# Kernel optimization log

Hardware: AMD Instinct MI355X
Metric: run time of the kernel (lower is better)

## Reference

```python
import jax, jax.numpy as jnp
import numpy as np

N = 16384      # total nodes (B graphs x 64 squares)
B = 256        # number of graphs
NODES = 64     # nodes per graph (chess board)
E = 131072     # directed edges (avg degree 8)
F_IN = 128
H = 256
GH = 4         # GAT heads
TH = 8         # transformer heads
L_GNN = 8
L_TF = 6
EPS = 1e-5


def layer_norm(x, g, b):
    m = jnp.mean(x, -1, keepdims=True)
    v = jnp.mean((x - m) ** 2, -1, keepdims=True)
    return (x - m) * jax.lax.rsqrt(v + EPS) * g + b


def setup_inputs() -> dict:
    key = jax.random.key(0)
    ks = iter(jax.random.split(key, 80))

    def nrm(shape, s=0.02):
        return jax.random.normal(next(ks), shape, jnp.float32) * s

    x = jax.random.normal(next(ks), (N, F_IN), jnp.float32)
    gid = jax.random.randint(next(ks), (E,), 0, B)
    off = jax.random.randint(next(ks), (2, E), 0, NODES)
    edge_index = gid[None, :] * NODES + off          # edges stay within a graph
    batch = jnp.arange(N, dtype=jnp.int32) // NODES
    piece_types = jax.random.randint(next(ks), (N,), 1, 7)
    return dict(
        x=x, edge_index=edge_index, batch=batch, piece_types=piece_types,
        emb_w=nrm((H, F_IN)), emb_b=nrm((H,)),
        gat_w=nrm((L_GNN, GH * H, H)), gat_as=nrm((L_GNN, GH, H)),
        gat_ad=nrm((L_GNN, GH, H)), gat_b=nrm((L_GNN, H)),
        gnn_g=jnp.ones((L_GNN, H)), gnn_beta=jnp.zeros((L_GNN, H)),
        ln1_g=jnp.ones((L_TF, H)), ln1_b=jnp.zeros((L_TF, H)),
        in_w=nrm((L_TF, 3 * H, H)), in_b=nrm((L_TF, 3 * H)),
        out_w=nrm((L_TF, H, H)), out_b=nrm((L_TF, H)),
        ln2_g=jnp.ones((L_TF, H)), ln2_b=jnp.zeros((L_TF, H)),
        ff1_w=nrm((L_TF, 4 * H, H)), ff1_b=nrm((L_TF, 4 * H)),
        ff2_w=nrm((L_TF, H, 4 * H)), ff2_b=nrm((L_TF, H)),
        pool_w=nrm((H,)), pool_b=nrm((1,)),
        vw1=nrm((H, H)), vb1=nrm((H,)), vw2=nrm((1, H)), vb2=nrm((1,)),
        pw1=nrm((H, H)), pb1=nrm((H,)), pw2=nrm((H, H)), pb2=nrm((H,)),
        uw1=nrm((H // 2, H)), ub1=nrm((H // 2,)), uw2=nrm((1, H // 2)), ub2=nrm((1,)))


def _forward(x, edge_index, batch, emb_w, emb_b, gat_w, gat_as, gat_ad, gat_b,
             gnn_g, gnn_beta, ln1_g, ln1_b, in_w, in_b, out_w, out_b, ln2_g,
             ln2_b, ff1_w, ff1_b, ff2_w, ff2_b, pool_w, pool_b, vw1, vb1, vw2,
             vb2, pw1, pb1, pw2, pb2, uw1, ub1, uw2, ub2):
    loops = jnp.arange(N, dtype=edge_index.dtype)     # GATConv add_self_loops=True
    src = jnp.concatenate([edge_index[0], loops])
    dst = jnp.concatenate([edge_index[1], loops])
    h = x @ emb_w.T + emb_b                           # [N,H] node embedding

    def gnn_layer(h, p):                              # ResidualGNNLayer
        W, a_s, a_d, bias, g, beta = p
        hp = (h @ W.T).reshape(N, GH, H)              # per-head projection
        al_s = jnp.sum(hp * a_s, -1)                  # [N,GH]
        al_d = jnp.sum(hp * a_d, -1)
        e = jax.nn.leaky_relu(al_s[src] + al_d[dst], 0.2)
        m = jax.ops.segment_max(e, dst, num_segments=N)
        ex = jnp.exp(e - m[dst])                      # segment softmax over dst
        den = jax.ops.segment_sum(ex, dst, num_segments=N)
        alpha = ex / den[dst]
        out = jax.ops.segment_sum(hp[src] * alpha[:, :, None], dst, num_segments=N)
        out = out.mean(1) + bias                      # concat=False -> head mean
        out = jax.nn.gelu(layer_norm(out, g, beta), approximate=False)
        return h + out, None                          # project = Identity

    h, _ = jax.lax.scan(gnn_layer, h, (gat_w, gat_as, gat_ad, gat_b, gnn_g, gnn_beta))

    # nn.MultiheadAttention defaults batch_first=False: axis0 (=B graphs) is the
    # sequence axis, axis1 (=64 nodes) is the batch axis — faithful to the source.
    xt = h.reshape(B, NODES, H)
    HD = H // TH

    def tf_layer(t, p):
        g1, b1, iw, ib, ow, ob, g2, b2, w1, fb1, w2, fb2 = p
        tn = layer_norm(t, g1, b1)
        q, k, v = jnp.split(tn @ iw.T + ib, 3, axis=-1)
        q = q.reshape(B, NODES, TH, HD)
        k = k.reshape(B, NODES, TH, HD)
        v = v.reshape(B, NODES, TH, HD)
        att = jnp.einsum('sbhd,tbhd->bhst', q, k) * (1.0 / HD ** 0.5)
        att = jax.nn.softmax(att, -1)
        o = jnp.einsum('bhst,tbhd->sbhd', att, v).reshape(B, NODES, H)
        t = t + (o @ ow.T + ob)
        tn = layer_norm(t, g2, b2)
        ff = jax.nn.gelu(tn @ w1.T + fb1, approximate=False) @ w2.T + fb2
        return t + ff, None

    xt, _ = jax.lax.scan(tf_layer, xt, (ln1_g, ln1_b, in_w, in_b, out_w, out_b,
                                        ln2_g, ln2_b, ff1_w, ff1_b, ff2_w, ff2_b))
    h = xt.reshape(N, H)

    # global attention pooling: softmax over ALL nodes (dim=0, as in the source)
    aw = jax.nn.softmax(h @ pool_w + pool_b[0], axis=0)
    g_rep = jax.ops.segment_sum(h * aw[:, None], batch, num_segments=B)
    value = jnp.tanh(jax.nn.gelu(g_rep @ vw1.T + vb1, approximate=False) @ vw2.T + vb2)[:, 0]
    policy = jax.nn.gelu(h @ pw1.T + pb1, approximate=False) @ pw2.T + pb2
    unc = jax.nn.softplus(jax.nn.gelu(g_rep @ uw1.T + ub1, approximate=False) @ uw2.T + ub2)[:, 0]
    return value, policy, unc


def reference(x, edge_index, batch, piece_types, emb_w, emb_b, gat_w, gat_as,
              gat_ad, gat_b, gnn_g, gnn_beta, ln1_g, ln1_b, in_w, in_b, out_w,
              out_b, ln2_g, ln2_b, ff1_w, ff1_b, ff2_w, ff2_b, pool_w, pool_b,
              vw1, vb1, vw2, vb2, pw1, pb1, pw2, pb2, uw1, ub1, uw2, ub2):
    # piece_types feeds PositionSpecificFeatureExtractor whose output is dead
    # code in the source forward (never used), so it is omitted here.
    return _forward(x, edge_index, batch, emb_w, emb_b, gat_w, gat_as, gat_ad,
                    gat_b, gnn_g, gnn_beta, ln1_g, ln1_b, in_w, in_b, out_w,
                    out_b, ln2_g, ln2_b, ff1_w, ff1_b, ff2_w, ff2_b, pool_w,
                    pool_b, vw1, vb1, vw2, vb2, pw1, pb1, pw2, pb2, uw1, ub1,
                    uw2, ub2)
```

## Files before the change

kernel.cpp:

```cpp
#include <hip/hip_runtime.h>
#include <hip/hip_bf16.h>

typedef __hip_bfloat16 bf16;
typedef __bf16 bf16x8 __attribute__((ext_vector_type(8)));
typedef float  f32x4  __attribute__((ext_vector_type(4)));

#define N_NODES 16384
#define HDIM    256
#define NE      131072
#define NE2     147456

__device__ __forceinline__ float b2f(bf16 v){ return __bfloat162float(v); }
__device__ __forceinline__ bf16  f2b(float v){ return __float2bfloat16(v); }
__device__ __forceinline__ float us2f(unsigned short u){
  union { unsigned int i; float f; } c; c.i = ((unsigned int)u) << 16; return c.f;
}
__device__ __forceinline__ unsigned short f2us(float f){
  bf16 h = __float2bfloat16(f);
  unsigned short u; __builtin_memcpy(&u, &h, 2); return u;
}
__device__ __forceinline__ float gelu_f(float x){
  return 0.5f * x * (1.0f + erff(x * 0.7071067811865476f));
}
__device__ __forceinline__ float wave_sum(float v){
  #pragma unroll
  for (int o = 32; o > 0; o >>= 1) v += __shfl_xor(v, o);
  return v;
}
__device__ __forceinline__ float wave_max(float v){
  #pragma unroll
  for (int o = 32; o > 0; o >>= 1) v = fmaxf(v, __shfl_xor(v, o));
  return v;
}

__device__ __forceinline__ float4 load4(const float* p){ return *(const float4*)p; }
__device__ __forceinline__ float4 load4(const bf16* p){
  ushort4 u = *(const ushort4*)p;
  return make_float4(us2f(u.x), us2f(u.y), us2f(u.z), us2f(u.w));
}
__device__ __forceinline__ void store4(float* p, float4 v){ *(float4*)p = v; }
__device__ __forceinline__ void store4(bf16* p, float4 v){
  ushort4 u = make_ushort4(f2us(v.x), f2us(v.y), f2us(v.z), f2us(v.w));
  *(ushort4*)p = u;
}
__device__ __forceinline__ void storev(float* p, float4 v){ *(float4*)p = v; }
__device__ __forceinline__ void storev(bf16*  p, float4 v){ store4(p, v); }

__device__ __forceinline__ void async_ld16(const bf16* g, unsigned short* l){
  __builtin_amdgcn_global_load_lds(
      (const __attribute__((address_space(1))) void*)g,
      (__attribute__((address_space(3))) void*)l, 16, 0, 0);
}

__global__ void detect_dtype(const unsigned short* __restrict__ x, int n, int* __restrict__ flags){
  int i = blockIdx.x * 256 + threadIdx.x;
  if (i < n) {
    unsigned short u = x[i];
    if ((u & 0x7F80) == 0x7F80) atomicOr(&flags[1], 1);
  }
}
struct ConvArgs {
  const void* src[35];
  unsigned short* dst[35];
  int cumg[36];
  int n[35];
};
__global__ void conv_all4(ConvArgs a, const int* __restrict__ flags){
  int gi = blockIdx.x * 256 + threadIdx.x;
  if (gi >= a.cumg[35]) return;
  int lo = 0, hi = 34;
  while (lo < hi) { int mid = (lo + hi + 1) >> 1; if (gi >= a.cumg[mid]) lo = mid; else hi = mid - 1; }
  int e0 = (gi - a.cumg[lo]) << 2;
  int n = a.n[lo];
  unsigned short* d = a.dst[lo];
  if (flags[1]) {
    const float* s = (const float*)a.src[lo];
    if (e0 + 4 <= n) {
      float4 v = *(const float4*)(s + e0);
      *(ushort4*)(d + e0) = make_ushort4(f2us(v.x), f2us(v.y), f2us(v.z), f2us(v.w));
    } else {
      for (int t = 0; t < n - e0; ++t) d[e0 + t] = f2us(s[e0 + t]);
    }
  } else {
    const unsigned short* s = (const unsigned short*)a.src[lo];
    if (e0 + 4 <= n) *(ushort4*)(d + e0) = *(const ushort4*)(s + e0);
    else for (int t = 0; t < n - e0; ++t) d[e0 + t] = s[e0 + t];
  }
}
__global__ void emit_out(const unsigned short* __restrict__ stage, void* __restrict__ out,
                         int n, const int* __restrict__ flags){
  int i = blockIdx.x * 256 + threadIdx.x;
  if (i >= n) return;
  if (flags[1]) ((float*)out)[i] = us2f(stage[i]);
  else          ((unsigned short*)out)[i] = stage[i];
}
__global__ void write_sentinel(bf16* out, float v){ out[threadIdx.x] = f2b(v); }

#define GF_GELU 1
#define GF_RES  2
#define GF_MIR  4
#define GF_ALS  8

template<typename TO, int FLAGS>
__global__ __launch_bounds__(256) void gemm2(
    const bf16* __restrict__ A, const bf16* __restrict__ W,
    const bf16* __restrict__ bias, const float* __restrict__ res,
    TO* __restrict__ C, bf16* __restrict__ C2, int M, int Nn, int K,
    const bf16* __restrict__ asp, const bf16* __restrict__ adp,
    float* __restrict__ alsp)
{
  __shared__ __align__(16) char ldsraw[36864];
  unsigned short* sA = (unsigned short*)ldsraw;
  unsigned short* sB = sA + 128 * 64;
  const int tid = threadIdx.x;
  const int wave = tid >> 6, lane = tid & 63;
  const int quad = lane >> 4, l16 = lane & 15;
  const int wm = wave & 1, wn = wave >> 1;
  const int row0 = blockIdx.y << 7, col0 = blockIdx.x << 7;
  const int lr = lane >> 3, lc = lane & 7;

  f32x4 acc[4][4] = {};

  for (int kt = 0; kt < K; kt += 64) {
    #pragma unroll
    for (int it = 0; it < 4; ++it) {
      int r0 = (wave << 5) + (it << 3);
      int rr = r0 + lr;
      int gch = lc ^ (rr & 7);
      async_ld16(A + (size_t)(row0 + rr) * K + kt + (gch << 3), sA + (r0 << 6));
      async_ld16(W + (size_t)(col0 + rr) * K + kt + (gch << 3), sB + (r0 << 6));
    }
    __syncthreads();
    #pragma unroll
    for (int kk = 0; kk < 2; ++kk) {
      bf16x8 af[4];
      #pragma unroll
      for (int i = 0; i < 4; ++i) {
        int m = (wm << 6) + (i << 4) + l16;
        af[i] = *(const bf16x8*)&sA[(m << 6) + ((((kk << 2) + quad) ^ (l16 & 7)) << 3)];
      }
      #pragma unroll
      for (int j = 0; j < 4; ++j) {
        int n = (wn << 6) + (j << 4) + l16;
        bf16x8 bfr = *(const bf16x8*)&sB[(n << 6) + ((((kk << 2) + quad) ^ (l16 & 7)) << 3)];
        #pragma unroll
        for (int i = 0; i < 4; ++i)
          acc[i][j] = __builtin_amdgcn_mfma_f32_16x16x32_bf16(af[i], bfr, acc[i][j], 0, 0, 0);
      }
    }
    __syncthreads();
  }

  float* ct = (float*)ldsraw + wave * (64 * 36);
  #pragma unroll
  for (int p = 0; p < 2; ++p) {
    #pragma unroll
    for (int i = 0; i < 4; ++i)
      #pragma unroll
      for (int r = 0; r < 4; ++r) {
        int row = (i << 4) + (quad << 2) + r;
        ct[row * 36 + l16]      = acc[i][(p << 1) + 0][r];
        ct[row * 36 + 16 + l16] = acc[i][(p << 1) + 1][r];
      }
    float4 sS = make_float4(0.f, 0.f, 0.f, 0.f);
    float4 sD = make_float4(0.f, 0.f, 0.f, 0.f);
    #pragma unroll
    for (int it2 = 0; it2 < 8; ++it2) {
      int row = (it2 << 3) + lr;
      int c4 = lc << 2;
      float4 v = *(const float4*)&ct[row * 36 + c4];
      int gcol = col0 + (wn << 6) + (p << 5) + c4;
      size_t gidx = (size_t)(row0 + (wm << 6) + row) * Nn + gcol;
      if (FLAGS & GF_ALS) {
        float asv = b2f(asp[row0 + (wm << 6) + row]);
        float adv = b2f(adp[row0 + (wm << 6) + row]);
        sS.x += asv * v.x; sS.y += asv * v.y; sS.z += asv * v.z; sS.w += asv * v.w;
        sD.x += adv * v.x; sD.y += adv * v.y; sD.z += adv * v.z; sD.w += adv * v.w;
      }
      if (bias) {
        float4 bv = load4(bias + gcol);
        v.x += bv.x; v.y += bv.y; v.z += bv.z; v.w += bv.w;
      }
      if (FLAGS & GF_GELU) {
        v.x = gelu_f(v.x); v.y = gelu_f(v.y); v.z = gelu_f(v.z); v.w = gelu_f(v.w);
      }
      if (FLAGS & GF_RES) {
        float4 rv = *(const float4*)&res[gidx];
        v.x += rv.x; v.y += rv.y; v.z += rv.z; v.w += rv.w;
      }
      storev(C + gidx, v);
      if (FLAGS & GF_MIR) store4(C2 + gidx, v);
    }
    if (FLAGS & GF_ALS) {
      #pragma unroll
      for (int o = 8; o < 64; o <<= 1) {
        sS.x += __shfl_xor(sS.x, o); sS.y += __shfl_xor(sS.y, o);
        sS.z += __shfl_xor(sS.z, o); sS.w += __shfl_xor(sS.w, o);
        sD.x += __shfl_xor(sD.x, o); sD.y += __shfl_xor(sD.y, o);
        sD.z += __shfl_xor(sD.z, o); sD.w += __shfl_xor(sD.w, o);
      }
      if (lr == 0) {
        int node = col0 + (wn << 6) + (p << 5) + (lc << 2);
        int hd2 = blockIdx.y >> 1;
        int slice = ((blockIdx.y & 1) << 1) | wm;
        *(float4*)&alsp[(size_t)((slice << 3) + hd2) * Nn + node] = sS;
        *(float4*)&alsp[(size_t)((slice << 3) + 4 + hd2) * Nn + node] = sD;
      }
    }
  }
}

template<bool POOL>
__global__ __launch_bounds__(256) void gemm_rln(
    const bf16* __restrict__ A, const bf16* __restrict__ W,
    const bf16* __restrict__ bias, float* __restrict__ h,
    bf16* __restrict__ tn, const bf16* __restrict__ lng,
    const bf16* __restrict__ lnb, int K,
    bf16* __restrict__ hbm, const bf16* __restrict__ pw,
    const bf16* __restrict__ pbp, float* __restrict__ logits)
{
  __shared__ __align__(16) char ldsraw[36864];
  unsigned short* sA = (unsigned short*)ldsraw;
  unsigned short* sB = sA + 32 * 64;
  const int tid = threadIdx.x;
  const int wave = tid >> 6, lane = tid & 63;
  const int quad = lane >> 4, l16 = lane & 15;
  const int row0 = blockIdx.x << 5;
  const int lr = lane >> 3, lc = lane & 7;

  f32x4 acc[2][4] = {};

  for (int kt = 0; kt < K; kt += 64) {
    {
      int rr = (wave << 3) + lr;
      int gch = lc ^ (rr & 7);
      async_ld16(A + (size_t)(row0 + rr) * K + kt + (gch << 3), sA + (wave << 9));
    }
    #pragma unroll
    for (int it = 0; it < 8; ++it) {
      int r0 = (wave << 6) + (it << 3);
      int rr = r0 + lr;
      int gch = lc ^ (rr & 7);
      async_ld16(W + (size_t)rr * K + kt + (gch << 3), sB + (r0 << 6));
    }
    __syncthreads();
    #pragma unroll
    for (int kk = 0; kk < 2; ++kk) {
      bf16x8 af[2];
      #pragma unroll
      for (int i = 0; i < 2; ++i) {
        int m = (i << 4) + l16;
        af[i] = *(const bf16x8*)&sA[(m << 6) + ((((kk << 2) + quad) ^ (l16 & 7)) << 3)];
      }
      #pragma unroll
      for (int j = 0; j < 4; ++j) {
        int n = (wave << 6) + (j << 4) + l16;
        bf16x8 bfr = *(const bf16x8*)&sB[(n << 6) + ((((kk << 2) + quad) ^ (l16 & 7)) << 3)];
        #pragma unroll
        for (int i = 0; i < 2; ++i)
          acc[i][j] = __builtin_amdgcn_mfma_f32_16x16x32_bf16(af[i], bfr, acc[i][j], 0, 0, 0);
      }
    }
    __syncthreads();
  }

  float* ct = (float*)ldsraw;
  #pragma unroll
  for (int j = 0; j < 4; ++j) {
    int col = (wave << 6) + (j << 4) + l16;
    #pragma unroll
    for (int i = 0; i < 2; ++i)
      #pragma unroll
      for (int r = 0; r < 4; ++r)
        ct[((i << 4) + (quad << 2) + r) * 260 + col] = acc[i][j][r];
  }
  __syncthreads();

  const int row = tid >> 3, q = tid & 7;
  const int c0 = q << 5;
  size_t gr = (size_t)(row0 + row) * 256 + c0;
  float4 v[8];
  float s1 = 0.f;
  #pragma unroll
  for (int k = 0; k < 8; ++k) {
    float4 cv = *(const float4*)&ct[row * 260 + c0 + (k << 2)];
    float4 bv = load4(bias + c0 + (k << 2));
    float4 rv = *(const float4*)&h[gr + (k << 2)];
    v[k].x = cv.x + bv.x + rv.x;
    v[k].y = cv.y + bv.y + rv.y;
    v[k].z = cv.z + bv.z + rv.z;
    v[k].w = cv.w + bv.w + rv.w;
    *(float4*)&h[gr + (k << 2)] = v[k];
    if (POOL) store4(hbm + gr + (k << 2), v[k]);
    s1 += v[k].x + v[k].y + v[k].z + v[k].w;
  }
  if (POOL) {
    float dp = 0.f;
    #pragma unroll
    for (int k = 0; k < 8; ++k) {
      float4 wv = load4(pw + c0 + (k << 2));
      dp += v[k].x * wv.x + v[k].y * wv.y + v[k].z * wv.z + v[k].w * wv.w;
    }
    dp += __shfl_xor(dp, 1); dp += __shfl_xor(dp, 2); dp += __shfl_xor(dp, 4);
    if (q == 0) logits[row0 + row] = dp + b2f(pbp[0]);
  } else {
    s1 += __shfl_xor(s1, 1); s1 += __shfl_xor(s1, 2); s1 += __shfl_xor(s1, 4);
    float mean = s1 * (1.0f / 256.0f);
    float s2 = 0.f;
    #pragma unroll
    for (int k = 0; k < 8; ++k) {
      float dx = v[k].x - mean, dy = v[k].y - mean, dz = v[k].z - mean, dw = v[k].w - mean;
      s2 += dx * dx + dy * dy + dz * dz + dw * dw;
    }
    s2 += __shfl_xor(s2, 1); s2 += __shfl_xor(s2, 2); s2 += __shfl_xor(s2, 4);
    float rstd = rsqrtf(s2 * (1.0f / 256.0f) + 1e-5f);
    #pragma unroll
    for (int k = 0; k < 8; ++k) {
      float4 gv = load4(lng + c0 + (k << 2));
      float4 bv2 = load4(lnb + c0 + (k << 2));
      float4 y;
      y.x = (v[k].x - mean) * rstd * gv.x + bv2.x;
      y.y = (v[k].y - mean) * rstd * gv.y + bv2.y;
      y.z = (v[k].z - mean) * rstd * gv.z + bv2.z;
      y.w = (v[k].w - mean) * rstd * gv.w + bv2.w;
      store4(tn + gr + (k << 2), y);
    }
  }
}

__global__ void csr_count(const int* __restrict__ edst, int* __restrict__ cnt){
  int e = blockIdx.x * 256 + threadIdx.x;
  if (e < NE2) {
    int d = (e < NE) ? edst[e] : (e - NE);
    atomicAdd(&cnt[d], 1);
  }
}
__global__ __launch_bounds__(1024) void csr_scan(const int* __restrict__ cnt, int* __restrict__ off){
  __shared__ int ls[1024];
  int t = threadIdx.x;
  int base = t * 16;
  int loc[16]; int s = 0;
  #pragma unroll
  for (int j = 0; j < 16; ++j) { loc[j] = s; s += cnt[base + j]; }
  ls[t] = s;
  __syncthreads();
  for (int o = 1; o < 1024; o <<= 1) {
    int v = (t >= o) ? ls[t - o] : 0;
    __syncthreads();
    ls[t] += v;
    __syncthreads();
  }
  int pre = (t == 0) ? 0 : ls[t - 1];
  #pragma unroll
  for (int j = 0; j < 16; ++j) off[base + j] = pre + loc[j];
  if (t == 1023) off[N_NODES] = ls[1023];
}
__global__ void csr_fill(const int* __restrict__ edst, const int* __restrict__ off,
                         int* __restrict__ fillc, int* __restrict__ list){
  int e = blockIdx.x * 256 + threadIdx.x;
  if (e < NE2) {
    int d = (e < NE) ? edst[e] : (e - NE);
    int p = atomicAdd(&fillc[d], 1);
    list[off[d] + p] = e;
  }
}

#define ALF_S 68

__device__ __forceinline__ bf16x8 pack8(const float* v, float scale){
  unsigned short u[8];
  #pragma unroll
  for (int t = 0; t < 8; ++t) u[t] = f2us(v[t] * scale);
  bf16x8 r; __builtin_memcpy(&r, u, 16); return r;
}

__global__ __launch_bounds__(256) void gat_graph2(
    const int* __restrict__ esrc, const bf16* __restrict__ hpT_g,
    const int* __restrict__ off, const int* __restrict__ list,
    const float* __restrict__ alsp,
    bf16* __restrict__ msg4, int g0, int hn)
{
  __shared__ unsigned short hpT[256 * 64];
  __shared__ float alpha[64 * ALF_S];
  __shared__ float als[64], ald[64], dinv[64];

  const int hd = blockIdx.x & 3;
  const int lg = blockIdx.x >> 2;
  const int g  = g0 + lg;
  const int tid = threadIdx.x;
  const int wave = tid >> 6, lane = tid & 63;
  const int quad = lane >> 4, l16 = lane & 15;
  const int nd = tid >> 2;
  const int k4 = tid & 3;

  {
    const int rl = lane >> 3, jj = lane & 7;
    #pragma unroll
    for (int it = 0; it < 8; ++it) {
      int c = (it << 5) + (wave << 3) + rl;
      async_ld16(hpT_g + (size_t)((hd << 8) + c) * 16384 + (g << 6) + ((jj ^ (c & 7)) << 3),
                 hpT + (((it << 5) + (wave << 3)) << 6));
    }
  }
  if (tid < 128) {
    int n2 = tid & 63;
    int sd = (tid >> 6) << 2;
    float v = 0.f;
    #pragma unroll
    for (int sl = 0; sl < 4; ++sl)
      v += alsp[(size_t)((sl << 3) + sd + hd) * 16384 + (g << 6) + n2];
    if (sd) ald[n2] = v; else als[n2] = v;
  }
  #pragma unroll
  for (int idx = tid; idx < 64 * ALF_S; idx += 256) alpha[idx] = 0.f;
  __syncthreads();

  {
    int st = off[(g << 6) + nd];
    int deg = off[(g << 6) + nd + 1] - st;
    float ad = ald[nd];
    float mx = -1e30f;
    for (int e = k4; e < deg; e += 4) {
      int ed = list[st + e];
      int sl = ((ed < NE) ? esrc[ed] : (ed - NE)) - (g << 6);
      float v = als[sl] + ad;
      v = (v > 0.f) ? v : 0.2f * v;
      mx = fmaxf(mx, v);
    }
    mx = fmaxf(mx, __shfl_xor(mx, 1)); mx = fmaxf(mx, __shfl_xor(mx, 2));
    float den = 0.f;
    for (int e = k4; e < deg; e += 4) {
      int ed = list[st + e];
      int sl = ((ed < NE) ? esrc[ed] : (ed - NE)) - (g << 6);
      float v = als[sl] + ad;
      v = (v > 0.f) ? v : 0.2f * v;
      float w = __expf(v - mx);
      den += w;
      atomicAdd(&alpha[nd * ALF_S + sl], w);
    }
    den += __shfl_xor(den, 1); den += __shfl_xor(den, 2);
    if (k4 == 0) dinv[nd] = 1.0f / den;
  }
  __syncthreads();

  f32x4 acc[4][4] = {};
  #pragma unroll
  for (int kk = 0; kk < 2; ++kk) {
    bf16x8 af[4];
    #pragma unroll
    for (int i = 0; i < 4; ++i) {
      int m = (i << 4) + l16;
      const float* ap = &alpha[m * ALF_S + (kk << 5) + (quad << 3)];
      float av[8];
      float4 a0 = *(const float4*)ap, a1 = *(const float4*)(ap + 4);
      av[0]=a0.x; av[1]=a0.y; av[2]=a0.z; av[3]=a0.w;
      av[4]=a1.x; av[5]=a1.y; av[6]=a1.z; av[7]=a1.w;
      af[i] = pack8(av, dinv[m]);
    }
    #pragma unroll
    for (int j = 0; j < 4; ++j) {
      int c2 = (wave << 6) + (j << 4) + l16;
      int chunk = (kk << 2) + quad;
      bf16x8 bfr = *(const bf16x8*)&hpT[(c2 << 6) + ((chunk ^ (c2 & 7)) << 3)];
      #pragma unroll
      for (int i = 0; i < 4; ++i)
        acc[i][j] = __builtin_amdgcn_mfma_f32_16x16x32_bf16(af[i], bfr, acc[i][j], 0, 0, 0);
    }
  }

  #pragma unroll
  for (int j = 0; j < 4; ++j) {
    int col = (wave << 6) + (j << 4) + l16;
    #pragma unroll
    for (int i = 0; i < 4; ++i) {
      int rbase = (i << 4) + (quad << 2);
      #pragma unroll
      for (int r = 0; r < 4; ++r)
        msg4[((size_t)hd * hn + (lg << 6) + rbase + r) * 256 + col] = f2b(acc[i][j][r]);
    }
  }
}

__global__ __launch_bounds__(256) void gat_epi(
    const bf16* __restrict__ msg4, int hn, int n0,
    const bf16* __restrict__ bias, const bf16* __restrict__ gg, const bf16* __restrict__ gb,
    float* __restrict__ h, bf16* __restrict__ hb,
    const bf16* __restrict__ lng, const bf16* __restrict__ lnb, bf16* __restrict__ tno)
{
  int nl = blockIdx.x * 4 + (threadIdx.x >> 6);
  int lane = threadIdx.x & 63;
  int c = lane * 4;
  float4 s = make_float4(0.f, 0.f, 0.f, 0.f);
  #pragma unroll
  for (int hd = 0; hd < 4; ++hd) {
    float4 m = load4(msg4 + ((size_t)hd * hn + nl) * 256 + c);
    s.x += m.x; s.y += m.y; s.z += m.z; s.w += m.w;
  }
  float4 bv = load4(bias + c);
  float ox = s.x * 0.25f + bv.x, oy = s.y * 0.25f + bv.y;
  float oz = s.z * 0.25f + bv.z, ow = s.w * 0.25f + bv.w;
  float mean = wave_sum(ox + oy + oz + ow) * (1.0f / 256.0f);
  float dx = ox - mean, dy = oy - mean, dz = oz - mean, dw = ow - mean;
  float var = wave_sum(dx*dx + dy*dy + dz*dz + dw*dw) * (1.0f / 256.0f);
  float r = rsqrtf(var + 1e-5f);
  float4 gv = load4(gg + c); float4 b2 = load4(gb + c);
  size_t base = ((size_t)(n0 + nl)) * 256 + c;
  float4 hv = load4(h + base);
  hv.x += gelu_f(dx * r * gv.x + b2.x);
  hv.y += gelu_f(dy * r * gv.y + b2.y);
  hv.z += gelu_f(dz * r * gv.z + b2.z);
  hv.w += gelu_f(dw * r * gv.w + b2.w);
  store4(h + base, hv);
  store4(hb + base, hv);
  if (lng) {
    float m2 = wave_sum(hv.x + hv.y + hv.z + hv.w) * (1.0f / 256.0f);
    float ex = hv.x - m2, ey = hv.y - m2, ez = hv.z - m2, ew = hv.w - m2;
    float v2 = wave_sum(ex*ex + ey*ey + ez*ez + ew*ew) * (1.0f / 256.0f);
    float r2 = rsqrtf(v2 + 1e-5f);
    float4 g2 = load4(lng + c); float4 bb = load4(lnb + c);
    store4(tno + base, make_float4(ex*r2*g2.x + bb.x, ey*r2*g2.y + bb.y,
                                   ez*r2*g2.z + bb.z, ew*r2*g2.w + bb.w));
  }
}

__global__ __launch_bounds__(256) void ln_kernel(
    const float* __restrict__ x, bf16* __restrict__ y,
    const bf16* __restrict__ g, const bf16* __restrict__ b)
{
  int row = blockIdx.x * 4 + (threadIdx.x >> 6);
  int lane = threadIdx.x & 63;
  int c = lane * 4;
  float4 v = load4(x + (size_t)row * 256 + c);
  float mean = wave_sum(v.x + v.y + v.z + v.w) * (1.0f / 256.0f);
  float dx = v.x - mean, dy = v.y - mean, dz = v.z - mean, dw = v.w - mean;
  float var = wave_sum(dx*dx + dy*dy + dz*dz + dw*dw) * (1.0f / 256.0f);
  float r = rsqrtf(var + 1e-5f);
  float4 gv = load4(g + c); float4 bv = load4(b + c);
  store4(y + (size_t)row * 256 + c,
         make_float4(dx*r*gv.x + bv.x, dy*r*gv.y + bv.y, dz*r*gv.z + bv.z, dw*r*gv.w + bv.w));
}

#define VT_LDS 268
#define P_LDS  72

__global__ __launch_bounds__(256) void attn_mfma(
    const bf16* __restrict__ qkv, bf16* __restrict__ obuf)
{
  const int b  = blockIdx.x & 63;
  const int hh = blockIdx.x >> 6;
  __shared__ unsigned short VTs[32 * VT_LDS];
  __shared__ unsigned short Ps[4][64 * P_LDS];
  const int tid  = threadIdx.x;
  const int wave = tid >> 6, lane = tid & 63;
  const int quad = lane >> 4, l16 = lane & 15;

  {
    const bf16* vb = qkv + (size_t)(tid * 64 + b) * 768 + 512 + hh * 32;
    unsigned short vv[32];
    *(uint4*)&vv[0]  = *(const uint4*)(vb);
    *(uint4*)&vv[8]  = *(const uint4*)(vb + 8);
    *(uint4*)&vv[16] = *(const uint4*)(vb + 16);
    *(uint4*)&vv[24] = *(const uint4*)(vb + 24);
    #pragma unroll
    for (int d = 0; d < 32; ++d) VTs[d * VT_LDS + tid] = vv[d];
  }
  bf16x8 qf[4];
  #pragma unroll
  for (int i = 0; i < 4; ++i) {
    int s = (wave << 6) + (i << 4) + l16;
    qf[i] = *(const bf16x8*)(qkv + (size_t)(s * 64 + b) * 768 + hh * 32 + (quad << 3));
  }
  __syncthreads();

  const float scale = 0.17677669529663687f;
  f32x4 oacc[4][2] = {};
  float lsum[4][4] = {};
  unsigned short* Pw = &Ps[wave][0];

  for (int nt = 0; nt < 4; ++nt) {
    bf16x8 kf[4];
    #pragma unroll
    for (int j = 0; j < 4; ++j) {
      int t = (nt << 6) + (j << 4) + l16;
      kf[j] = *(const bf16x8*)(qkv + (size_t)(t * 64 + b) * 768 + 256 + hh * 32 + (quad << 3));
    }
    f32x4 zero = {0.f, 0.f, 0.f, 0.f};
    f32x4 sx[4][4];
    #pragma unroll
    for (int i = 0; i < 4; ++i)
      #pragma unroll
      for (int j = 0; j < 4; ++j)
        sx[i][j] = __builtin_amdgcn_mfma_f32_16x16x32_bf16(qf[i], kf[j], zero, 0, 0, 0);
    #pragma unroll
    for (int i = 0; i < 4; ++i) {
      #pragma unroll
      for (int r = 0; r < 4; ++r) {
        float p[4]; float rs = 0.f;
        #pragma unroll
        for (int j = 0; j < 4; ++j) {
          float sc = fminf(fmaxf(sx[i][j][r] * scale, -60.f), 60.f);
          p[j] = __expf(sc);
          rs += p[j];
        }
        #pragma unroll
        for (int o = 1; o < 16; o <<= 1) rs += __shfl_xor(rs, o);
        lsum[i][r] += rs;
        int row = (i << 4) + (quad << 2) + r;
        #pragma unroll
        for (int j = 0; j < 4; ++j)
          Pw[row * P_LDS + (j << 4) + l16] = f2us(p[j]);
      }
    }
    #pragma unroll
    for (int kk = 0; kk < 2; ++kk) {
      bf16x8 vf[2];
      #pragma unroll
      for (int j2 = 0; j2 < 2; ++j2)
        vf[j2] = *(const bf16x8*)&VTs[((j2 << 4) + l16) * VT_LDS + (nt << 6) + (kk << 5) + (quad << 3)];
      #pragma unroll
      for (int i2 = 0; i2 < 4; ++i2) {
        bf16x8 pf = *(const bf16x8*)&Pw[((i2 << 4) + l16) * P_LDS + (kk << 5) + (quad << 3)];
        #pragma unroll
        for (int j2 = 0; j2 < 2; ++j2)
          oacc[i2][j2] = __builtin_amdgcn_mfma_f32_16x16x32_bf16(pf, vf[j2], oacc[i2][j2], 0, 0, 0);
      }
    }
  }
  #pragma unroll
  for (int i = 0; i < 4; ++i) {
    #pragma unroll
    for (int r = 0; r < 4; ++r) {
      int srow = (wave << 6) + (i << 4) + (quad << 2) + r;
      float inv = 1.0f / lsum[i][r];
      #pragma unroll
      for (int j2 = 0; j2 < 2; ++j2)
        obuf[(size_t)(srow * 64 + b) * 256 + hh * 32 + (j2 << 4) + l16] = f2b(oacc[i][j2][r] * inv);
    }
  }
}

__global__ __launch_bounds__(1024) void pool_reduce(
    const float* __restrict__ logits, float* __restrict__ red)
{
  __shared__ float sm[16];
  int t = threadIdx.x;
  float m = -1e30f;
  for (int i = t; i < N_NODES; i += 1024) m = fmaxf(m, logits[i]);
  m = wave_max(m);
  if ((t & 63) == 0) sm[t >> 6] = m;
  __syncthreads();
  if (t == 0) { float mm = sm[0]; for (int i = 1; i < 16; ++i) mm = fmaxf(mm, sm[i]); sm[0] = mm; }
  __syncthreads();
  float gmax = sm[0];
  __syncthreads();
  float s = 0.f;
  for (int i = t; i < N_NODES; i += 1024) s += expf(logits[i] - gmax);
  s = wave_sum(s);
  if ((t & 63) == 0) sm[t >> 6] = s;
  __syncthreads();
  if (t == 0) { float ss = 0.f; for (int i = 0; i < 16; ++i) ss += sm[i]; red[0] = gmax; red[1] = 1.0f / ss; }
}
__global__ __launch_bounds__(256) void pool_grep(
    const float* __restrict__ h, const float* __restrict__ logits,
    const float* __restrict__ red, bf16* __restrict__ g_rep)
{
  __shared__ float w[64];
  int g = blockIdx.x; int tid = threadIdx.x;
  if (tid < 64) w[tid] = expf(logits[g * 64 + tid] - red[0]) * red[1];
  __syncthreads();
  float acc = 0.f;
  for (int nd = 0; nd < 64; ++nd) acc += h[((size_t)g * 64 + nd) * 256 + tid] * w[nd];
  g_rep[(size_t)g * 256 + tid] = f2b(acc);
}
__global__ __launch_bounds__(256) void head_value(
    const float* __restrict__ vt, const bf16* __restrict__ w2, const bf16* __restrict__ b2,
    bf16* __restrict__ out)
{
  int gidx = blockIdx.x * 4 + (threadIdx.x >> 6); int lane = threadIdx.x & 63;
  float acc = 0.f;
  #pragma unroll
  for (int j = 0; j < 4; ++j) { int c = j * 64 + lane; acc += vt[(size_t)gidx * 256 + c] * b2f(w2[c]); }
  acc = wave_sum(acc);
  if (lane == 0) out[gidx] = f2b(tanhf(acc + b2f(b2[0])));
}
__global__ __launch_bounds__(256) void head_unc(
    const float* __restrict__ ut, const bf16* __restrict__ w2, const bf16* __restrict__ b2,
    bf16* __restrict__ out)
{
  int gidx = blockIdx.x * 4 + (threadIdx.x >> 6); int lane = threadIdx.x & 63;
  float acc = 0.f;
  #pragma unroll
  for (int j = 0; j < 2; ++j) { int c = j * 64 + lane; acc += ut[(size_t)gidx * 128 + c] * b2f(w2[c]); }
  acc = wave_sum(acc);
  if (lane == 0) {
    float x = acc + b2f(b2[0]);
    float sp = (x > 20.f) ? x : log1pf(expf(x));
    out[gidx] = f2b(sp);
  }
}

extern "C" void kernel_launch(void* const* d_in, const int* in_sizes, int n_in,
                              void* d_out, int out_size, void* d_ws, size_t ws_size,
                              hipStream_t stream)
{
  (void)out_size;
  const int* eidx = (const int*)d_in[1];

  char* ws = (char*)d_ws;
  size_t wo = 0;
  auto alloc = [&](size_t bytes) -> char* {
    char* p = ws + wo; wo += (bytes + 255) & ~(size_t)255; return p;
  };
  int*   flags = (int*)alloc(256);
  int*   cnt   = (int*)alloc((size_t)N_NODES * 4);
  int*   fillc = (int*)alloc((size_t)N_NODES * 4);
  size_t zero_end = wo;

  bf16* conv[38] = {};
  static const int fidx[35] = {0,4,5,6,7,8,9,10,11,12,13,14,15,16,17,18,19,
                               20,21,22,23,24,25,26,27,28,29,30,31,32,33,34,35,36,37};
  for (int j = 0; j < 35; ++j) {
    int idx = fidx[j];
    conv[idx] = (bf16*)alloc((size_t)in_sizes[idx] * 2);
  }
  float* h     = (float*)alloc((size_t)N_NODES * 256 * 4);
  bf16*  hb    = (bf16*) alloc((size_t)N_NODES * 256 * 2);
  bf16*  big   = (bf16*) alloc((size_t)N_NODES * 1024 * 2);
  const int OUT_ELEMS = 256 + N_NODES * 256 + 256;
  bf16*  tn     = (bf16*)alloc((size_t)N_NODES * 256 * 2);
  bf16*  ostage = (bf16*)alloc((size_t)OUT_ELEMS * 2);
  int*   off   = (int*)alloc((size_t)(N_NODES + 1) * 4);
  int*   list  = (int*)alloc((size_t)NE2 * 4);
  float* logits= (float*)alloc((size_t)N_NODES * 4);
  float* redb  = (float*)alloc(256);
  bf16*  g_rep = (bf16*)alloc((size_t)256 * 256 * 2);
  float* val_t = (float*)alloc((size_t)256 * 256 * 4);
  float* unc_t = (float*)alloc((size_t)256 * 128 * 4);
  float* alsp  = (float*)alloc((size_t)32 * N_NODES * 4);
  size_t base_needed = wo;

  if (n_in != 38)                   { write_sentinel<<<1,256,0,stream>>>((bf16*)d_out, 4.f);  return; }
  if (in_sizes[0] != N_NODES * 128) { write_sentinel<<<1,256,0,stream>>>((bf16*)d_out, 8.f);  return; }
  if (in_sizes[1] != 2 * NE)        { write_sentinel<<<1,256,0,stream>>>((bf16*)d_out, 16.f); return; }
  if (ws_size < base_needed)        { write_sentinel<<<1,256,0,stream>>>((bf16*)d_out, 32.f); return; }

  size_t msg_bytes = (size_t)4 * N_NODES * 256 * 2;
  bf16* msg4; int halves;
  if (ws_size >= base_needed + msg_bytes + 256) {
    msg4 = (bf16*)alloc(msg_bytes); halves = 1;
  } else {
    msg4 = tn; halves = 2;
  }

  hipMemsetAsync(d_ws, 0, zero_end, stream);

  detect_dtype<<<256, 256, 0, stream>>>((const unsigned short*)d_in[0], 65536, flags);
  {
    ConvArgs ca;
    int cum = 0;
    for (int j = 0; j < 35; ++j) {
      int idx = fidx[j];
      ca.src[j] = d_in[idx];
      ca.dst[j] = (unsigned short*)conv[idx];
      ca.cumg[j] = cum;
      ca.n[j] = in_sizes[idx];
      cum += (in_sizes[idx] + 3) >> 2;
    }
    ca.cumg[35] = cum;
    conv_all4<<<(cum + 255) / 256, 256, 0, stream>>>(ca, flags);
  }
  const bf16 *xb = conv[0], *emb_w = conv[4], *emb_b = conv[5], *gat_w = conv[6],
             *gat_as = conv[7], *gat_ad = conv[8], *gat_b = conv[9], *gnn_g = conv[10],
             *gnn_beta = conv[11], *ln1_g = conv[12], *ln1_b = conv[13], *in_w = conv[14],
             *in_b = conv[15], *out_w = conv[16], *out_b = conv[17], *ln2_g = conv[18],
             *ln2_b = conv[19], *ff1_w = conv[20], *ff1_b = conv[21], *ff2_w = conv[22],
             *ff2_b = conv[23], *pool_w = conv[24], *pool_b = conv[25],
             *vw1 = conv[26], *vb1 = conv[27], *vw2 = conv[28], *vb2 = conv[29],
             *pw1 = conv[30], *pb1 = conv[31], *pw2 = conv[32], *pb2 = conv[33],
             *uw1 = conv[34], *ub1 = conv[35], *uw2 = conv[36], *ub2 = conv[37];

  bf16* qkv  = big;
  bf16* obuf = big + (size_t)N_NODES * 768;
  bf16* hpT_g = big;
  bf16* ffb  = big;
  bf16* o_val = ostage;
  bf16* o_pol = ostage + 256;
  bf16* o_unc = ostage + 256 + (size_t)N_NODES * 256;

  csr_count<<<(NE2 + 255) / 256, 256, 0, stream>>>(eidx + NE, cnt);
  csr_scan<<<1, 1024, 0, stream>>>(cnt, off);
  csr_fill<<<(NE2 + 255) / 256, 256, 0, stream>>>(eidx + NE, off, fillc, list);

  gemm2<float, GF_MIR><<<dim3(2, 128), 256, 0, stream>>>(
      xb, emb_w, emb_b, nullptr, h, hb, N_NODES, 256, 128,
      nullptr, nullptr, nullptr);

  const int gph = 256 / halves;
  const int hn  = N_NODES / halves;
  for (int l = 0; l < 8; ++l) {
    gemm2<bf16, GF_ALS><<<dim3(128, 8), 256, 0, stream>>>(
        gat_w + (size_t)l * 1024 * 256, hb, nullptr, nullptr, hpT_g, nullptr,
        1024, N_NODES, 256, gat_as + l * 1024, gat_ad + l * 1024, alsp);
    const bf16* lng = (l == 7 && halves == 1) ? ln1_g : nullptr;
    const bf16* lnb = (l == 7 && halves == 1) ? ln1_b : nullptr;
    for (int ph = 0; ph < halves; ++ph) {
      gat_graph2<<<gph * 4, 256, 0, stream>>>(eidx, hpT_g, off, list, alsp,
          msg4, ph * gph, hn);
      gat_epi<<<hn / 4, 256, 0, stream>>>(msg4, hn, ph * hn,
          gat_b + l * 256, gnn_g + l * 256, gnn_beta + l * 256, h, hb,
          lng, lnb, tn);
    }
  }
  if (halves == 2)
    ln_kernel<<<N_NODES / 4, 256, 0, stream>>>(h, tn, ln1_g, ln1_b);

  for (int l = 0; l < 6; ++l) {
    gemm2<bf16, 0><<<dim3(6, 128), 256, 0, stream>>>(
        tn, in_w + (size_t)l * 768 * 256, in_b + l * 768, nullptr, qkv, nullptr, N_NODES, 768, 256,
        nullptr, nullptr, nullptr);
    attn_mfma<<<512, 256, 0, stream>>>(qkv, obuf);
    gemm_rln<false><<<N_NODES / 32, 256, 0, stream>>>(
        obuf, out_w + (size_t)l * 256 * 256, out_b + l * 256, h, tn,
        ln2_g + l * 256, ln2_b + l * 256, 256,
        nullptr, nullptr, nullptr, nullptr);
    gemm2<bf16, GF_GELU><<<dim3(8, 128), 256, 0, stream>>>(
        tn, ff1_w + (size_t)l * 1024 * 256, ff1_b + l * 1024, nullptr, ffb, nullptr, N_NODES, 1024, 256,
        nullptr, nullptr, nullptr);
    if (l < 5)
      gemm_rln<false><<<N_NODES / 32, 256, 0, stream>>>(
          ffb, ff2_w + (size_t)l * 256 * 1024, ff2_b + l * 256, h, tn,
          ln1_g + (l + 1) * 256, ln1_b + (l + 1) * 256, 1024,
          nullptr, nullptr, nullptr, nullptr);
    else
      gemm_rln<true><<<N_NODES / 32, 256, 0, stream>>>(
          ffb, ff2_w + (size_t)l * 256 * 1024, ff2_b + l * 256, h, nullptr,
          nullptr, nullptr, 1024,
          hb, pool_w, pool_b, logits);
  }

  pool_reduce<<<1, 1024, 0, stream>>>(logits, redb);
  pool_grep<<<256, 256, 0, stream>>>(h, logits, redb, g_rep);
  gemm2<float, GF_GELU><<<dim3(2, 2), 256, 0, stream>>>(
      g_rep, vw1, vb1, nullptr, val_t, nullptr, 256, 256, 256,
      nullptr, nullptr, nullptr);
  head_value<<<64, 256, 0, stream>>>(val_t, vw2, vb2, o_val);
  gemm2<float, GF_GELU><<<dim3(1, 2), 256, 0, stream>>>(
      g_rep, uw1, ub1, nullptr, unc_t, nullptr, 256, 128, 256,
      nullptr, nullptr, nullptr);
  head_unc<<<64, 256, 0, stream>>>(unc_t, uw2, ub2, o_unc);
  gemm2<bf16, GF_GELU><<<dim3(2, 128), 256, 0, stream>>>(
      hb, pw1, pb1, nullptr, tn, nullptr, N_NODES, 256, 256,
      nullptr, nullptr, nullptr);
  gemm2<bf16, 0><<<dim3(2, 128), 256, 0, stream>>>(
      tn, pw2, pb2, nullptr, o_pol, nullptr, N_NODES, 256, 256,
      nullptr, nullptr, nullptr);

  emit_out<<<(OUT_ELEMS + 255) / 256, 256, 0, stream>>>(
      (const unsigned short*)ostage, d_out, OUT_ELEMS, flags);
}
```

Measured before the change: 1.501 ms.

## Fuse policy MLP and value/uncertainty heads; remap GEMM block order

Replaces the two policy-head GEMM launches with one kernel that keeps the GELU intermediate in shared memory, so the 16384x256 intermediate no longer goes through global memory. Merges the value and uncertainty MLPs, including their final dot products, into a single small kernel, which removes four launches and two temporary buffers. Also permutes block indices in gemm2 and gemm_rln so consecutive blocks are spread across row tiles, intended to improve cache locality or distribution across XCDs. The added shared-memory footprint in gemm_pol may lower occupancy.

```diff
diff --git a/kernel.cpp b/kernel.cpp
--- a/kernel.cpp
+++ b/kernel.cpp
@@ -116,7 +116,16 @@
   const int wave = tid >> 6, lane = tid & 63;
   const int quad = lane >> 4, l16 = lane & 15;
   const int wm = wave & 1, wn = wave >> 1;
-  const int row0 = blockIdx.y << 7, col0 = blockIdx.x << 7;
+  int bx = blockIdx.x, by = blockIdx.y;
+  {
+    int gx = gridDim.x, tot = gx * gridDim.y;
+    if ((tot & 7) == 0) {
+      int flat = by * gx + bx, q8 = tot >> 3;
+      int nf = (flat & 7) * q8 + (flat >> 3);
+      bx = nf % gx; by = nf / gx;
+    }
+  }
+  const int row0 = by << 7, col0 = bx << 7;
   const int lr = lane >> 3, lc = lane & 7;
 
   f32x4 acc[4][4] = {};
@@ -201,8 +210,8 @@
       }
       if (lr == 0) {
         int node = col0 + (wn << 6) + (p << 5) + (lc << 2);
-        int hd2 = blockIdx.y >> 1;
-        int slice = ((blockIdx.y & 1) << 1) | wm;
+        int hd2 = by >> 1;
+        int slice = ((by & 1) << 1) | wm;
         *(float4*)&alsp[(size_t)((slice << 3) + hd2) * Nn + node] = sS;
         *(float4*)&alsp[(size_t)((slice << 3) + 4 + hd2) * Nn + node] = sD;
       }
@@ -225,7 +234,10 @@
   const int tid = threadIdx.x;
   const int wave = tid >> 6, lane = tid & 63;
   const int quad = lane >> 4, l16 = lane & 15;
-  const int row0 = blockIdx.x << 5;
+  int bid = blockIdx.x;
+  { int tot = gridDim.x;
+    if ((tot & 7) == 0) { int q8 = tot >> 3; bid = (bid & 7) * q8 + (bid >> 3); } }
+  const int row0 = bid << 5;
   const int lr = lane >> 3, lc = lane & 7;
 
   f32x4 acc[2][4] = {};
@@ -324,6 +336,266 @@
       y.z = (v[k].z - mean) * rstd * gv.z + bv2.z;
       y.w = (v[k].w - mean) * rstd * gv.w + bv2.w;
       store4(tn + gr + (k << 2), y);
+    }
+  }
+}
+
+__global__ __launch_bounds__(256) void gemm_pol(
+    const bf16* __restrict__ A, const bf16* __restrict__ W1,
+    const bf16* __restrict__ b1, const bf16* __restrict__ W2,
+    const bf16* __restrict__ b2p, bf16* __restrict__ out)
+{
+  __shared__ __align__(16) char ldsraw[36864];
+  __shared__ __align__(16) unsigned short inter[4][2048];
+  unsigned short* sA = (unsigned short*)ldsraw;
+  unsigned short* sB = sA + 32 * 64;
+  const int tid = threadIdx.x;
+  const int wave = tid >> 6, lane = tid & 63;
+  const int quad = lane >> 4, l16 = lane & 15;
+  int bid = blockIdx.x;
+  { int tot = gridDim.x;
+    if ((tot & 7) == 0) { int q8 = tot >> 3; bid = (bid & 7) * q8 + (bid >> 3); } }
+  const int row0 = bid << 5;
+  const int lr = lane >> 3, lc = lane & 7;
+  float* ct = (float*)ldsraw;
+  const int row = tid >> 3, q = tid & 7;
+  const int c0 = q << 5;
+
+  {
+    f32x4 acc[2][4] = {};
+    for (int kt = 0; kt < 256; kt += 64) {
+      { int rr = (wave << 3) + lr; int gch = lc ^ (rr & 7);
+        async_ld16(A + (size_t)(row0 + rr) * 256 + kt + (gch << 3), sA + (wave << 9)); }
+      #pragma unroll
+      for (int it = 0; it < 8; ++it) {
+        int r0 = (wave << 6) + (it << 3); int rr = r0 + lr; int gch = lc ^ (rr & 7);
+        async_ld16(W1 + (size_t)rr * 256 + kt + (gch << 3), sB + (r0 << 6));
+      }
+      __syncthreads();
+      #pragma unroll
+      for (int kk = 0; kk < 2; ++kk) {
+        bf16x8 af[2];
+        #pragma unroll
+        for (int i = 0; i < 2; ++i) {
+          int m = (i << 4) + l16;
+          af[i] = *(const bf16x8*)&sA[(m << 6) + ((((kk << 2) + quad) ^ (l16 & 7)) << 3)];
+        }
+        #pragma unroll
+        for (int j = 0; j < 4; ++j) {
+          int n = (wave << 6) + (j << 4) + l16;
+          bf16x8 bfr = *(const bf16x8*)&sB[(n << 6) + ((((kk << 2) + quad) ^ (l16 & 7)) << 3)];
+          #pragma unroll
+          for (int i = 0; i < 2; ++i)
+            acc[i][j] = __builtin_amdgcn_mfma_f32_16x16x32_bf16(af[i], bfr, acc[i][j], 0, 0, 0);
+        }
+      }
+      __syncthreads();
+    }
+    #pragma unroll
+    for (int j = 0; j < 4; ++j) {
+      int col = (wave << 6) + (j << 4) + l16;
+      #pragma unroll
+      for (int i = 0; i < 2; ++i)
+        #pragma unroll
+        for (int r = 0; r < 4; ++r)
+          ct[((i << 4) + (quad << 2) + r) * 260 + col] = acc[i][j][r];
+    }
+    __syncthreads();
+    #pragma unroll
+    for (int k = 0; k < 8; ++k) {
+      int col = c0 + (k << 2);
+      float4 cv = *(const float4*)&ct[row * 260 + col];
+      float4 bv = load4(b1 + col);
+      unsigned short u[4] = { f2us(gelu_f(cv.x + bv.x)), f2us(gelu_f(cv.y + bv.y)),
+                              f2us(gelu_f(cv.z + bv.z)), f2us(gelu_f(cv.w + bv.w)) };
+      int ktb = col >> 6, cc = col & 63, ch = cc >> 3, wc = cc & 7;
+      *(ushort4*)&inter[ktb][(row << 6) + ((ch ^ (row & 7)) << 3) + wc] = *(ushort4*)u;
+    }
+  }
+  __syncthreads();
+
+  {
+    f32x4 acc[2][4] = {};
+    #pragma unroll
+    for (int kt2 = 0; kt2 < 4; ++kt2) {
+      #pragma unroll
+      for (int it = 0; it < 8; ++it) {
+        int r0 = (wave << 6) + (it << 3); int rr = r0 + lr; int gch = lc ^ (rr & 7);
+        async_ld16(W2 + (size_t)rr * 256 + (kt2 << 6) + (gch << 3), sB + (r0 << 6));
+      }
+      __syncthreads();
+      #pragma unroll
+      for (int kk = 0; kk < 2; ++kk) {
+        bf16x8 af[2];
+        #pragma unroll
+        for (int i = 0; i < 2; ++i) {
+          int m = (i << 4) + l16;
+          af[i] = *(const bf16x8*)&inter[kt2][(m << 6) + ((((kk << 2) + quad) ^ (l16 & 7)) << 3)];
+        }
+        #pragma unroll
+        for (int j = 0; j < 4; ++j) {
+          int n = (wave << 6) + (j << 4) + l16;
+          bf16x8 bfr = *(const bf16x8*)&sB[(n << 6) + ((((kk << 2) + quad) ^ (l16 & 7)) << 3)];
+          #pragma unroll
+          for (int i = 0; i < 2; ++i)
+            acc[i][j] = __builtin_amdgcn_mfma_f32_16x16x32_bf16(af[i], bfr, acc[i][j], 0, 0, 0);
+        }
+      }
+      __syncthreads();
+    }
+    #pragma unroll
+    for (int j = 0; j < 4; ++j) {
+      int col = (wave << 6) + (j << 4) + l16;
+      #pragma unroll
+      for (int i = 0; i < 2; ++i)
+        #pragma unroll
+        for (int r = 0; r < 4; ++r)
+          ct[((i << 4) + (quad << 2) + r) * 260 + col] = acc[i][j][r];
+    }
+    __syncthreads();
+    #pragma unroll
+    for (int k = 0; k < 8; ++k) {
+      int col = c0 + (k << 2);
+      float4 cv = *(const float4*)&ct[row * 260 + col];
+      float4 bv = load4(b2p + col);
+      store4(out + (size_t)(row0 + row) * 256 + col,
+             make_float4(cv.x + bv.x, cv.y + bv.y, cv.z + bv.z, cv.w + bv.w));
+    }
+  }
+}
+
+__global__ __launch_bounds__(256) void heads_fused(
+    const bf16* __restrict__ g_rep,
+    const bf16* __restrict__ vw1, const bf16* __restrict__ vb1,
+    const bf16* __restrict__ vw2, const bf16* __restrict__ vb2,
+    const bf16* __restrict__ uw1, const bf16* __restrict__ ub1,
+    const bf16* __restrict__ uw2, const bf16* __restrict__ ub2,
+    bf16* __restrict__ o_val, bf16* __restrict__ o_unc)
+{
+  __shared__ __align__(16) char ldsraw[36864];
+  unsigned short* sA = (unsigned short*)ldsraw;
+  unsigned short* sB = sA + 32 * 64;
+  const int tid = threadIdx.x;
+  const int wave = tid >> 6, lane = tid & 63;
+  const int quad = lane >> 4, l16 = lane & 15;
+  const int row0 = blockIdx.x << 5;
+  const int lr = lane >> 3, lc = lane & 7;
+  float* ct = (float*)ldsraw;
+  const int row = tid >> 3, q = tid & 7;
+  const int c0 = q << 5;
+
+  {
+    f32x4 acc[2][4] = {};
+    for (int kt = 0; kt < 256; kt += 64) {
+      { int rr = (wave << 3) + lr; int gch = lc ^ (rr & 7);
+        async_ld16(g_rep + (size_t)(row0 + rr) * 256 + kt + (gch << 3), sA + (wave << 9)); }
+      #pragma unroll
+      for (int it = 0; it < 8; ++it) {
+        int r0 = (wave << 6) + (it << 3); int rr = r0 + lr; int gch = lc ^ (rr & 7);
+        async_ld16(vw1 + (size_t)rr * 256 + kt + (gch << 3), sB + (r0 << 6));
+      }
+      __syncthreads();
+      #pragma unroll
+      for (int kk = 0; kk < 2; ++kk) {
+        bf16x8 af[2];
+        #pragma unroll
+        for (int i = 0; i < 2; ++i) {
+          int m = (i << 4) + l16;
+          af[i] = *(const bf16x8*)&sA[(m << 6) + ((((kk << 2) + quad) ^ (l16 & 7)) << 3)];
+        }
+        #pragma unroll
+        for (int j = 0; j < 4; ++j) {
+          int n = (wave << 6) + (j << 4) + l16;
+          bf16x8 bfr = *(const bf16x8*)&sB[(n << 6) + ((((kk << 2) + quad) ^ (l16 & 7)) << 3)];
+          #pragma unroll
+          for (int i = 0; i < 2; ++i)
+            acc[i][j] = __builtin_amdgcn_mfma_f32_16x16x32_bf16(af[i], bfr, acc[i][j], 0, 0, 0);
+        }
+      }
+      __syncthreads();
+    }
+    #pragma unroll
+    for (int j = 0; j < 4; ++j) {
+      int col = (wave << 6) + (j << 4) + l16;
+      #pragma unroll
+      for (int i = 0; i < 2; ++i)
+        #pragma unroll
+        for (int r = 0; r < 4; ++r)
+          ct[((i << 4) + (quad << 2) + r) * 260 + col] = acc[i][j][r];
+    }
+    __syncthreads();
+    float dp = 0.f;
+    #pragma unroll
+    for (int k = 0; k < 8; ++k) {
+      float4 cv = *(const float4*)&ct[row * 260 + c0 + (k << 2)];
+      float4 bv = load4(vb1 + c0 + (k << 2));
+      float4 wv = load4(vw2 + c0 + (k << 2));
+      dp += gelu_f(cv.x + bv.x) * wv.x + gelu_f(cv.y + bv.y) * wv.y
+          + gelu_f(cv.z + bv.z) * wv.z + gelu_f(cv.w + bv.w) * wv.w;
+    }
+    dp += __shfl_xor(dp, 1); dp += __shfl_xor(dp, 2); dp += __shfl_xor(dp, 4);
+    if (q == 0) o_val[row0 + row] = f2b(tanhf(dp + b2f(vb2[0])));
+  }
+  __syncthreads();
+
+  {
+    f32x4 acc[2][4] = {};
+    for (int kt = 0; kt < 256; kt += 64) {
+      { int rr = (wave << 3) + lr; int gch = lc ^ (rr & 7);
+        async_ld16(g_rep + (size_t)(row0 + rr) * 256 + kt + (gch << 3), sA + (wave << 9)); }
+      #pragma unroll
+      for (int it = 0; it < 4; ++it) {
+        int r0 = (wave << 5) + (it << 3); int rr = r0 + lr; int gch = lc ^ (rr & 7);
+        async_ld16(uw1 + (size_t)rr * 256 + kt + (gch << 3), sB + (r0 << 6));
+      }
+      __syncthreads();
+      #pragma unroll
+      for (int kk = 0; kk < 2; ++kk) {
+        bf16x8 af[2];
+        #pragma unroll
+        for (int i = 0; i < 2; ++i) {
+          int m = (i << 4) + l16;
+          af[i] = *(const bf16x8*)&sA[(m << 6) + ((((kk << 2) + quad) ^ (l16 & 7)) << 3)];
+        }
+        #pragma unroll
+        for (int j = 0; j < 4; ++j) {
+          int n = ((wave & 1) << 6) + (j << 4) + l16;
+          bf16x8 bfr = *(const bf16x8*)&sB[(n << 6) + ((((kk << 2) + quad) ^ (l16 & 7)) << 3)];
+          #pragma unroll
+          for (int i = 0; i < 2; ++i)
+            acc[i][j] = __builtin_amdgcn_mfma_f32_16x16x32_bf16(af[i], bfr, acc[i][j], 0, 0, 0);
+        }
+      }
+      __syncthreads();
+    }
+    if (wave < 2) {
+      #pragma unroll
+      for (int j = 0; j < 4; ++j) {
+        int col = (wave << 6) + (j << 4) + l16;
+        #pragma unroll
+        for (int i = 0; i < 2; ++i)
+          #pragma unroll
+          for (int r = 0; r < 4; ++r)
+            ct[((i << 4) + (quad << 2) + r) * 260 + col] = acc[i][j][r];
+      }
+    }
+    __syncthreads();
+    float dp = 0.f;
+    if (q < 4) {
+      #pragma unroll
+      for (int k = 0; k < 8; ++k) {
+        float4 cv = *(const float4*)&ct[row * 260 + c0 + (k << 2)];
+        float4 bv = load4(ub1 + c0 + (k << 2));
+        float4 wv = load4(uw2 + c0 + (k << 2));
+        dp += gelu_f(cv.x + bv.x) * wv.x + gelu_f(cv.y + bv.y) * wv.y
+            + gelu_f(cv.z + bv.z) * wv.z + gelu_f(cv.w + bv.w) * wv.w;
+      }
+    }
+    dp += __shfl_xor(dp, 1); dp += __shfl_xor(dp, 2); dp += __shfl_xor(dp, 4);
+    if (q == 0) {
+      float x = dp + b2f(ub2[0]);
+      float sp = (x > 20.f) ? x : log1pf(expf(x));
+      o_unc[row0 + row] = f2b(sp);
     }
   }
 }
@@ -672,32 +944,6 @@
   for (int nd = 0; nd < 64; ++nd) acc += h[((size_t)g * 64 + nd) * 256 + tid] * w[nd];
   g_rep[(size_t)g * 256 + tid] = f2b(acc);
 }
-__global__ __launch_bounds__(256) void head_value(
-    const float* __restrict__ vt, const bf16* __restrict__ w2, const bf16* __restrict__ b2,
-    bf16* __restrict__ out)
-{
-  int gidx = blockIdx.x * 4 + (threadIdx.x >> 6); int lane = threadIdx.x & 63;
-  float acc = 0.f;
-  #pragma unroll
-  for (int j = 0; j < 4; ++j) { int c = j * 64 + lane; acc += vt[(size_t)gidx * 256 + c] * b2f(w2[c]); }
-  acc = wave_sum(acc);
-  if (lane == 0) out[gidx] = f2b(tanhf(acc + b2f(b2[0])));
-}
-__global__ __launch_bounds__(256) void head_unc(
-    const float* __restrict__ ut, const bf16* __restrict__ w2, const bf16* __restrict__ b2,
-    bf16* __restrict__ out)
-{
-  int gidx = blockIdx.x * 4 + (threadIdx.x >> 6); int lane = threadIdx.x & 63;
-  float acc = 0.f;
-  #pragma unroll
-  for (int j = 0; j < 2; ++j) { int c = j * 64 + lane; acc += ut[(size_t)gidx * 128 + c] * b2f(w2[c]); }
-  acc = wave_sum(acc);
-  if (lane == 0) {
-    float x = acc + b2f(b2[0]);
-    float sp = (x > 20.f) ? x : log1pf(expf(x));
-    out[gidx] = f2b(sp);
-  }
-}
 
 extern "C" void kernel_launch(void* const* d_in, const int* in_sizes, int n_in,
                               void* d_out, int out_size, void* d_ws, size_t ws_size,
@@ -734,8 +980,6 @@
   float* logits= (float*)alloc((size_t)N_NODES * 4);
   float* redb  = (float*)alloc(256);
   bf16*  g_rep = (bf16*)alloc((size_t)256 * 256 * 2);
-  float* val_t = (float*)alloc((size_t)256 * 256 * 4);
-  float* unc_t = (float*)alloc((size_t)256 * 128 * 4);
   float* alsp  = (float*)alloc((size_t)32 * N_NODES * 4);
   size_t base_needed = wo;
 
@@ -840,20 +1084,9 @@
 
   pool_reduce<<<1, 1024, 0, stream>>>(logits, redb);
   pool_grep<<<256, 256, 0, stream>>>(h, logits, redb, g_rep);
-  gemm2<float, GF_GELU><<<dim3(2, 2), 256, 0, stream>>>(
-      g_rep, vw1, vb1, nullptr, val_t, nullptr, 256, 256, 256,
-      nullptr, nullptr, nullptr);
-  head_value<<<64, 256, 0, stream>>>(val_t, vw2, vb2, o_val);
-  gemm2<float, GF_GELU><<<dim3(1, 2), 256, 0, stream>>>(
-      g_rep, uw1, ub1, nullptr, unc_t, nullptr, 256, 128, 256,
-      nullptr, nullptr, nullptr);
-  head_unc<<<64, 256, 0, stream>>>(unc_t, uw2, ub2, o_unc);
-  gemm2<bf16, GF_GELU><<<dim3(2, 128), 256, 0, stream>>>(
-      hb, pw1, pb1, nullptr, tn, nullptr, N_NODES, 256, 256,
-      nullptr, nullptr, nullptr);
-  gemm2<bf16, 0><<<dim3(2, 128), 256, 0, stream>>>(
-      tn, pw2, pb2, nullptr, o_pol, nullptr, N_NODES, 256, 256,
-      nullptr, nullptr, nullptr);
+  heads_fused<<<8, 256, 0, stream>>>(
+      g_rep, vw1, vb1, vw2, vb2, uw1, ub1, uw2, ub2, o_val, o_unc);
+  gemm_pol<<<N_NODES / 32, 256, 0, stream>>>(hb, pw1, pb1, pw2, pb2, o_pol);
 
   emit_out<<<(OUT_ELEMS + 255) / 256, 256, 0, stream>>>(
       (const unsigned short*)ostage, d_out, OUT_ELEMS, flags);
```

New measurement: 1.628 ms. 8.4% more time.
